# Kernel tuning notes

Hardware: AMD Instinct MI355X
Metric: run time of the kernel (lower is better)

Reference implementation:

```python
import jax, jax.numpy as jnp
import numpy as np
from jax import lax

B, C, H, W = 4, 256, 128, 128
NH = 8
HD = C // NH  # 32
K = 7         # toodd(7) -> 7
DIL = 2
NBH = K // 2  # neighborhood radius


def _window_start(i, L, k, d):
    nh = k // 2
    if d <= 1:
        return max(i - nh, 0) + (L - i - nh - 1 if i + nh >= L else 0)
    ni = i - nh * d
    if ni < 0:
        return i % d
    if i + nh * d >= L:
        imodd = i % d
        a = (L // d) * d
        b = L - a
        if imodd < b:
            return L - b + imodd - 2 * nh * d
        return a + imodd - k * d
    return ni


def _pb_start(i, L, k, d):
    nh = k // 2
    if d <= 1:
        return nh + (nh - i if i < nh else 0) + (L - i - 1 - nh if i + nh >= L else 0)
    if i - nh * d < 0:
        return k - 1 - (i // d)
    if i + nh * d >= L:
        return (L - i - 1) // d
    return nh


# [L, K] neighbor indices per axis, and [L] relative-position-bias start offsets
IDX_H = np.array([[_window_start(i, H, K, DIL) + ki * DIL for ki in range(K)] for i in range(H)], dtype=np.int32)
IDX_W = np.array([[_window_start(j, W, K, DIL) + kj * DIL for kj in range(K)] for j in range(W)], dtype=np.int32)
PB_H = np.array([_pb_start(i, H, K, DIL) for i in range(H)], dtype=np.int32)
PB_W = np.array([_pb_start(j, W, K, DIL) for j in range(W)], dtype=np.int32)


def setup_inputs() -> dict:
    key = jax.random.key(0)
    ks = jax.random.split(key, 8)
    gain = 2.0 ** (-2.5)
    x = jax.random.normal(ks[0], (B, C, H, W), jnp.float32)
    # rotary tables in [-1, 1]
    sin = jax.random.uniform(ks[1], (H, W, HD), jnp.float32, minval=-1.0, maxval=1.0)
    cos = jax.random.uniform(ks[2], (H, W, HD), jnp.float32, minval=-1.0, maxval=1.0)
    w_qkv = jax.random.normal(ks[3], (3 * C, C), jnp.float32) * gain * (2.0 / (4 * C)) ** 0.5
    b_qkv = jnp.zeros((3 * C,), jnp.float32)
    w_lepe = jax.random.normal(ks[4], (C, 1, 5, 5), jnp.float32) * 0.02
    b_lepe = jnp.zeros((C,), jnp.float32)
    w_proj = jax.random.normal(ks[5], (C, C), jnp.float32) * gain * (1.0 / C) ** 0.5
    b_proj = jnp.zeros((C,), jnp.float32)
    rpb = jax.random.normal(ks[6], (NH, 2 * K - 1, 2 * K - 1), jnp.float32) * 0.02
    return {"x": x, "sin": sin, "cos": cos, "w_qkv": w_qkv, "b_qkv": b_qkv,
            "w_lepe": w_lepe, "b_lepe": b_lepe, "w_proj": w_proj, "b_proj": b_proj, "rpb": rpb}


def _rotate_every_two(t):
    t1 = t[..., ::2]
    t2 = t[..., 1::2]
    return jnp.stack([-t2, t1], axis=-1).reshape(t.shape)


def _forward(x, sin, cos, w_qkv, b_qkv, w_lepe, b_lepe, w_proj, b_proj, rpb):
    Bx, Cx, Hx, Wx = x.shape
    # 1x1 qkv conv
    qkv = jnp.einsum('oc,bchw->bohw', w_qkv, x) + b_qkv[None, :, None, None]
    v_chan = qkv[:, 2 * Cx:]
    # LePE: depthwise 5x5 conv on v channels
    lepe = lax.conv_general_dilated(v_chan, w_lepe, (1, 1), [(2, 2), (2, 2)],
                                    feature_group_count=Cx,
                                    dimension_numbers=('NCHW', 'OIHW', 'NCHW'))
    lepe = lepe + b_lepe[None, :, None, None]

    def split_heads(t):  # [B, n*c, H, W] -> [B, n, H, W, c]
        return t.reshape(Bx, NH, HD, Hx, Wx).transpose(0, 1, 3, 4, 2)

    q = split_heads(qkv[:, :Cx])
    k = split_heads(qkv[:, Cx:2 * Cx])
    v = split_heads(v_chan)

    q = (q * cos + _rotate_every_two(q) * sin) * (HD ** -0.5)
    k = k * cos + _rotate_every_two(k) * sin

    idx_h = jnp.asarray(IDX_H)
    idx_w = jnp.asarray(IDX_W)
    pb_h = jnp.asarray(PB_H)
    pb_w = jnp.asarray(PB_W)

    # na2d_qk: dilated neighborhood scores + relative position bias
    attn_slices = []
    for ki in range(K):
        kh = jnp.take(k, idx_h[:, ki], axis=2)          # [B,n,H,W,c]
        for kj in range(K):
            khw = jnp.take(kh, idx_w[:, kj], axis=3)    # [B,n,H,W,c]
            s = jnp.einsum('bnhwc,bnhwc->bnhw', q, khw)
            bias = rpb[:, pb_h + ki][:, :, pb_w + kj]    # [n,H,W]
            attn_slices.append(s + bias[None])
    attn = jnp.stack(attn_slices, axis=-1)               # [B,n,H,W,K*K]
    attn = jax.nn.softmax(attn, axis=-1)

    # na2d_av
    out = jnp.zeros_like(v)
    idx = 0
    for ki in range(K):
        vh = jnp.take(v, idx_h[:, ki], axis=2)
        for kj in range(K):
            vhw = jnp.take(vh, idx_w[:, kj], axis=3)
            out = out + attn[..., idx, None] * vhw
            idx += 1

    out = out.transpose(0, 1, 4, 2, 3).reshape(Bx, Cx, Hx, Wx)  # merge heads
    out = out + lepe
    return jnp.einsum('oc,bchw->bohw', w_proj, out) + b_proj[None, :, None, None]


def reference(x, sin, cos, w_qkv, b_qkv, w_lepe, b_lepe, w_proj, b_proj, rpb):
    return _forward(x, sin, cos, w_qkv, b_qkv, w_lepe, b_lepe, w_proj, b_proj, rpb)
```

## Files before the change

### kernel.cpp

```cpp
#include <hip/hip_runtime.h>
#include <cstddef>

#define HW 16384
#define WID 128

typedef __attribute__((ext_vector_type(8))) short short8;
typedef __attribute__((ext_vector_type(4))) float f32x4;

#define GLD4(g, l)                                                        \
    __builtin_amdgcn_global_load_lds(                                     \
        (const __attribute__((address_space(1))) unsigned int*)(g),       \
        (__attribute__((address_space(3))) unsigned int*)(l), 4, 0, 0)

__device__ __forceinline__ int wstart(int i) {
    if (i < 6) return i & 1;
    if (i >= 122) return 114 + (i & 1);
    return i - 6;
}
__device__ __forceinline__ int pbstart(int i) {
    if (i < 6) return 6 - (i >> 1);
    if (i >= 122) return (127 - i) >> 1;
    return 3;
}

__device__ __forceinline__ unsigned short bf16rne(float f) {
    unsigned u = __builtin_bit_cast(unsigned, f);
    u += 0x7FFFu + ((u >> 16) & 1u);
    return (unsigned short)(u >> 16);
}
__device__ __forceinline__ void bsplit(float f, unsigned short& h, unsigned short& l) {
    h = bf16rne(f);
    float hf = __builtin_bit_cast(float, ((unsigned)h) << 16);
    l = bf16rne(f - hf);
}

template <bool QKV>
__global__ __launch_bounds__(256, 2) void gemm_mfma(
    const float* __restrict__ Wm, const float* __restrict__ Xf, size_t bstr,
    const float* __restrict__ bias, const float* __restrict__ sinp,
    const float* __restrict__ cosp, float* __restrict__ Y, int NMT, int MT) {
    __shared__ unsigned short As_h[128][40], As_l[128][40];
    __shared__ unsigned short Bs_h[128][40], Bs_l[128][40];
    const int bid = blockIdx.x;
    const int xcd = bid & 7, r = bid >> 3;
    const int mt = r % NMT;
    const int q2 = r / NMT;
    const int nt = xcd * 16 + (q2 & 15);
    const int b = q2 >> 4;
    const int t = threadIdx.x;
    const int lane = t & 63, wid = t >> 6;
    const int wm = wid >> 1, wn = wid & 1;
    const int m0 = mt * 128, n0 = nt * 128;

    f32x4 acc[4][4];
#pragma unroll
    for (int i = 0; i < 4; i++)
#pragma unroll
        for (int j = 0; j < 4; j++) acc[i][j] = (f32x4){0.f, 0.f, 0.f, 0.f};

    const int sr = t >> 1, sh = t & 1;
    const float* arow = Wm + (size_t)(m0 + sr) * 256 + sh * 16;
    const int pl = t & 127, khalf = (t >> 7) * 16;
    const float* xcol = Xf + (size_t)b * bstr + n0 + pl;

    for (int ks = 0; ks < 8; ks++) {
        {
            const float* ap = arow + ks * 32;
#pragma unroll
            for (int g = 0; g < 2; g++) {
                float4 f0 = *(const float4*)(ap + g * 8);
                float4 f1 = *(const float4*)(ap + g * 8 + 4);
                float ff[8] = {f0.x, f0.y, f0.z, f0.w, f1.x, f1.y, f1.z, f1.w};
                short8 vh, vl;
#pragma unroll
                for (int e = 0; e < 8; e++) {
                    unsigned short h, lo_;
                    bsplit(ff[e], h, lo_);
                    vh[e] = (short)h;
                    vl[e] = (short)lo_;
                }
                *(short8*)&As_h[sr][sh * 16 + g * 8] = vh;
                *(short8*)&As_l[sr][sh * 16 + g * 8] = vl;
            }
        }
        {
            const float* xc = xcol + (size_t)(ks * 32 + khalf) * HW;
            float vv[16];
#pragma unroll
            for (int e = 0; e < 16; e++) vv[e] = xc[(size_t)e * HW];
            short8 vh0, vh1, vl0, vl1;
#pragma unroll
            for (int e = 0; e < 8; e++) {
                unsigned short h, lo_;
                bsplit(vv[e], h, lo_);
                vh0[e] = (short)h;
                vl0[e] = (short)lo_;
                bsplit(vv[e + 8], h, lo_);
                vh1[e] = (short)h;
                vl1[e] = (short)lo_;
            }
            *(short8*)&Bs_h[pl][khalf] = vh0;
            *(short8*)&Bs_h[pl][khalf + 8] = vh1;
            *(short8*)&Bs_l[pl][khalf] = vl0;
            *(short8*)&Bs_l[pl][khalf + 8] = vl1;
        }
        __syncthreads();
        const int k8 = (lane >> 4) * 8;
        short8 a_h[4], a_l[4];
#pragma unroll
        for (int mi = 0; mi < 4; mi++) {
            int am = wm * 64 + mi * 16 + (lane & 15);
            a_h[mi] = *(const short8*)&As_h[am][k8];
            a_l[mi] = *(const short8*)&As_l[am][k8];
        }
#pragma unroll
        for (int ni = 0; ni < 4; ni++) {
            int bn = wn * 64 + ni * 16 + (lane & 15);
            short8 b_h = *(const short8*)&Bs_h[bn][k8];
            short8 b_l = *(const short8*)&Bs_l[bn][k8];
#pragma unroll
            for (int mi = 0; mi < 4; mi++) {
                acc[mi][ni] = __builtin_amdgcn_mfma_f32_16x16x32_bf16(a_h[mi], b_h, acc[mi][ni], 0, 0, 0);
                acc[mi][ni] = __builtin_amdgcn_mfma_f32_16x16x32_bf16(a_h[mi], b_l, acc[mi][ni], 0, 0, 0);
                acc[mi][ni] = __builtin_amdgcn_mfma_f32_16x16x32_bf16(a_l[mi], b_h, acc[mi][ni], 0, 0, 0);
            }
        }
        __syncthreads();
    }

    const int col = lane & 15, rq = (lane >> 4) * 4;
    const int s = QKV ? (mt >> 1) : 3;
#pragma unroll
    for (int mi = 0; mi < 4; mi++) {
        int mrow = m0 + wm * 64 + mi * 16 + rq;
        float b0 = bias[mrow], b1 = bias[mrow + 1], b2 = bias[mrow + 2], b3 = bias[mrow + 3];
#pragma unroll
        for (int ni = 0; ni < 4; ni++) {
            int p = n0 + wn * 64 + ni * 16 + col;
            float v0 = acc[mi][ni][0] + b0, v1 = acc[mi][ni][1] + b1;
            float v2 = acc[mi][ni][2] + b2, v3 = acc[mi][ni][3] + b3;
            if (QKV && s < 2) {
                int d0 = (mi & 1) * 16 + rq;
                const float* cp = cosp + (size_t)p * 32 + d0;
                const float* sp = sinp + (size_t)p * 32 + d0;
                float c0 = cp[0], c1 = cp[1], c2 = cp[2], c3 = cp[3];
                float s0 = sp[0], s1 = sp[1], s2 = sp[2], s3 = sp[3];
                float n0_ = v0 * c0 - v1 * s0, n1_ = v1 * c1 + v0 * s1;
                float n2_ = v2 * c2 - v3 * s2, n3_ = v3 * c3 + v2 * s3;
                if (s == 0) {
                    const float scl = 0.17677669529663687f;
                    n0_ *= scl; n1_ *= scl; n2_ *= scl; n3_ *= scl;
                }
                v0 = n0_; v1 = n1_; v2 = n2_; v3 = n3_;
            }
            float* yp = Y + ((size_t)b * MT + mrow) * HW + p;
            yp[0] = v0;
            yp[HW] = v1;
            yp[2 * HW] = v2;
            yp[3 * HW] = v3;
        }
    }
}

#define CW 2048
#define PBUF 4096
__global__ __launch_bounds__(256) void attn_k(const float* __restrict__ qkv,
                                              const float* __restrict__ rpb,
                                              const float* __restrict__ wl,
                                              const float* __restrict__ bl,
                                              float* __restrict__ out) {
    __shared__ float sm[2 * PBUF];
    const int t = threadIdx.x;
    const int ty = t >> 7;
    const int j = t & 127;
    const int bx = blockIdx.x;
    const int ip = ((bx & 7) << 3) | (bx >> 3);
    const int i0 = ip * 2;
    const int i = i0 + ty;
    const int n = blockIdx.y, b = blockIdx.z;
    const int r0 = wstart(i0);
    const int w64 = (t >> 6) * 64;

    const float* qb = qkv + ((size_t)b * 768 + n * 32) * HW;
    const float* kb = qb + (size_t)256 * HW;
    const float* vb = qb + (size_t)512 * HW;
    const int p = i * WID + j;
    const float* qrow = qb + i0 * WID;
    const float* krow = kb + r0 * WID;
    const float* vrow = vb + r0 * WID;

    const int hs = wstart(i), ws_ = wstart(j);
    const int ph = pbstart(i), pw = pbstart(j);

    float sc[49];
    const float* rp = rpb + n * 169;
#pragma unroll
    for (int ki = 0; ki < 7; ki++)
#pragma unroll
        for (int kj = 0; kj < 7; kj++)
            sc[ki * 7 + kj] = rp[(ph + ki) * 13 + (pw + kj)];

    const int aoff = (hs - r0) * WID + ws_;

#pragma unroll
    for (int s = 0; s < 2; s++) {
        const float* kp = krow + (size_t)s * HW;
#pragma unroll
        for (int u = 0; u < 7; u++) GLD4(kp + u * 256 + t, &sm[s * CW + u * 256 + w64]);
        GLD4(qrow + (size_t)s * HW + t, &sm[s * CW + 1792 + w64]);
    }

    for (int cp = 0; cp < 16; cp++) {
        float* bc = sm + (cp & 1) * PBUF;
        float* bnx = sm + ((cp + 1) & 1) * PBUF;
        if (cp < 15) {
#pragma unroll
            for (int s = 0; s < 2; s++) {
                const int c = 2 * (cp + 1) + s;
                const float* kp = krow + (size_t)c * HW;
#pragma unroll
                for (int u = 0; u < 7; u++) GLD4(kp + u * 256 + t, &bnx[s * CW + u * 256 + w64]);
                GLD4(qrow + (size_t)c * HW + t, &bnx[s * CW + 1792 + w64]);
            }
            asm volatile("s_waitcnt vmcnt(16)" ::: "memory");
        } else {
#pragma unroll
            for (int s = 0; s < 2; s++) {
                const float* vp = vrow + (size_t)s * HW;
#pragma unroll
                for (int u = 0; u < 7; u++) GLD4(vp + u * 256 + t, &bnx[s * CW + u * 256 + w64]);
            }
            asm volatile("s_waitcnt vmcnt(14)" ::: "memory");
        }
        __builtin_amdgcn_s_barrier();
        __builtin_amdgcn_s_setprio(1);
#pragma unroll
        for (int s = 0; s < 2; s++) {
            const float* bs = bc + s * CW;
            float qc = bs[1792 + t];
            const float* smb = bs + aoff;
#pragma unroll
            for (int ki = 0; ki < 7; ki++) {
                const float* kib = smb + ki * 256;
#pragma unroll
                for (int kj = 0; kj < 7; kj++)
                    sc[ki * 7 + kj] = fmaf(qc, kib[kj * 2], sc[ki * 7 + kj]);
            }
        }
        __builtin_amdgcn_s_setprio(0);
        __builtin_amdgcn_s_barrier();
    }

    float mx = sc[0];
#pragma unroll
    for (int u = 1; u < 49; u++) mx = fmaxf(mx, sc[u]);
    float sum = 0.0f;
#pragma unroll
    for (int u = 0; u < 49; u++) {
        sc[u] = __expf(sc[u] - mx);
        sum += sc[u];
    }
    float inv = 1.0f / sum;
#pragma unroll
    for (int u = 0; u < 49; u++) sc[u] *= inv;

    float* ob = out + ((size_t)b * 768 + n * 32) * HW + p;
    const float* wbase = wl + (size_t)(n * 32) * 25;
    const float* blb = bl + n * 32;
    for (int cp = 0; cp < 16; cp++) {
        float* bc = sm + (cp & 1) * PBUF;
        float* bnx = sm + ((cp + 1) & 1) * PBUF;
        if (cp < 15) {
#pragma unroll
            for (int s = 0; s < 2; s++) {
                const int c = 2 * (cp + 1) + s;
                const float* vp = vrow + (size_t)c * HW;
#pragma unroll
                for (int u = 0; u < 7; u++) GLD4(vp + u * 256 + t, &bnx[s * CW + u * 256 + w64]);
            }
            asm volatile("s_waitcnt vmcnt(14)" ::: "memory");
        } else {
            asm volatile("s_waitcnt vmcnt(0)" ::: "memory");
        }
        __builtin_amdgcn_s_barrier();
        __builtin_amdgcn_s_setprio(1);
#pragma unroll
        for (int s = 0; s < 2; s++) {
            const int ch = 2 * cp + s;
            const float* bs = bc + s * CW;
            const float* smb = bs + aoff;
            float oc = 0.0f;
#pragma unroll
            for (int ki = 0; ki < 7; ki++) {
                const float* kib = smb + ki * 256;
#pragma unroll
                for (int kj = 0; kj < 7; kj++)
                    oc = fmaf(sc[ki * 7 + kj], kib[kj * 2], oc);
            }
            const float* wrow = wbase + ch * 25;
            float lac = blb[ch];
#pragma unroll
            for (int di = 0; di < 5; di++) {
                int ii = i + di - 2;
                if ((unsigned)ii < 128u) {
                    const float* srow = bs + (ii - r0) * WID;
                    const float* wr = wrow + di * 5;
#pragma unroll
                    for (int dj = 0; dj < 5; dj++) {
                        int jj = j + dj - 2;
                        if ((unsigned)jj < 128u)
                            lac = fmaf(wr[dj], srow[jj], lac);
                    }
                }
            }
            ob[(size_t)ch * HW] = oc + lac;
        }
        __builtin_amdgcn_s_setprio(0);
        __builtin_amdgcn_s_barrier();
    }
}

extern "C" void kernel_launch(void* const* d_in, const int* in_sizes, int n_in,
                              void* d_out, int out_size, void* d_ws, size_t ws_size,
                              hipStream_t stream) {
    const float* x = (const float*)d_in[0];
    const float* sinp = (const float*)d_in[1];
    const float* cosp = (const float*)d_in[2];
    const float* w_qkv = (const float*)d_in[3];
    const float* b_qkv = (const float*)d_in[4];
    const float* w_lepe = (const float*)d_in[5];
    const float* b_lepe = (const float*)d_in[6];
    const float* w_proj = (const float*)d_in[7];
    const float* b_proj = (const float*)d_in[8];
    const float* rpb = (const float*)d_in[9];
    float* out = (float*)d_out;

    float* qkvb = (float*)d_ws;

    gemm_mfma<true><<<dim3(3072), 256, 0, stream>>>(w_qkv, x, (size_t)256 * HW, b_qkv,
                                                    sinp, cosp, qkvb, 6, 768);
    attn_k<<<dim3(64, 8, 4), 256, 0, stream>>>(qkvb, rpb, w_lepe, b_lepe, qkvb);
    gemm_mfma<false><<<dim3(1024), 256, 0, stream>>>(w_proj, qkvb, (size_t)768 * HW, b_proj,
                                                     nullptr, nullptr, out, 2, 256);
}
```

Before: 369.6 us.

## Compute two output rows per thread in attention kernel to reuse K/V window rows

The attention kernel now has each thread handle two query rows (i and i+2), so each block covers four rows and the grid halves. The staged K/V window grows from 7 to 8 rows, and rows shared by both dilated neighborhoods are loaded from LDS once and used for both accumulations. This applies to scores, PV and the LePE conv. Q is now read straight into registers instead of being staged through LDS. The cost is doubled score registers (98 floats) with a launch-bounds hint of 3 blocks per CU, which risks spills, plus half as many blocks; the bf16 split helper also switches to HIP intrinsics.

```diff
diff --git a/kernel.cpp b/kernel.cpp
--- a/kernel.cpp
+++ b/kernel.cpp
@@ -1,4 +1,5 @@
 #include <hip/hip_runtime.h>
+#include <hip/hip_bf16.h>
 #include <cstddef>
 
 #define HW 16384
@@ -23,15 +24,11 @@
     return 3;
 }
 
-__device__ __forceinline__ unsigned short bf16rne(float f) {
-    unsigned u = __builtin_bit_cast(unsigned, f);
-    u += 0x7FFFu + ((u >> 16) & 1u);
-    return (unsigned short)(u >> 16);
-}
 __device__ __forceinline__ void bsplit(float f, unsigned short& h, unsigned short& l) {
-    h = bf16rne(f);
-    float hf = __builtin_bit_cast(float, ((unsigned)h) << 16);
-    l = bf16rne(f - hf);
+    __hip_bfloat16 hb = __float2bfloat16(f);
+    h = __builtin_bit_cast(unsigned short, hb);
+    float hf = __bfloat162float(hb);
+    l = __builtin_bit_cast(unsigned short, __float2bfloat16(f - hf));
 }
 
 template <bool QKV>
@@ -162,158 +159,213 @@
     }
 }
 
-#define CW 2048
-#define PBUF 4096
-__global__ __launch_bounds__(256) void attn_k(const float* __restrict__ qkv,
-                                              const float* __restrict__ rpb,
-                                              const float* __restrict__ wl,
-                                              const float* __restrict__ bl,
-                                              float* __restrict__ out) {
-    __shared__ float sm[2 * PBUF];
+template <int O>
+__device__ __forceinline__ void qk2(const float* win, int aoff, float qA, float qB,
+                                    float (&sl)[49], float (&sh)[49]) {
+    const float* rw = win + aoff;
+#pragma unroll
+    for (int u = 0; u < 7 + O; u++) {
+        float tp[7];
+#pragma unroll
+        for (int kj = 0; kj < 7; kj++) tp[kj] = rw[kj * 2];
+        if (u < 7) {
+#pragma unroll
+            for (int kj = 0; kj < 7; kj++) sl[u * 7 + kj] = fmaf(qA, tp[kj], sl[u * 7 + kj]);
+        }
+        if (u >= O) {
+#pragma unroll
+            for (int kj = 0; kj < 7; kj++) sh[(u - O) * 7 + kj] = fmaf(qB, tp[kj], sh[(u - O) * 7 + kj]);
+        }
+        rw += 2 * WID;
+    }
+}
+
+template <int O>
+__device__ __forceinline__ void pv2(const float* win, int aoff, const float (&sl)[49],
+                                    const float (&sh)[49], float& oA, float& oB) {
+    const float* rw = win + aoff;
+#pragma unroll
+    for (int u = 0; u < 7 + O; u++) {
+        float tp[7];
+#pragma unroll
+        for (int kj = 0; kj < 7; kj++) tp[kj] = rw[kj * 2];
+        if (u < 7) {
+#pragma unroll
+            for (int kj = 0; kj < 7; kj++) oA = fmaf(sl[u * 7 + kj], tp[kj], oA);
+        }
+        if (u >= O) {
+#pragma unroll
+            for (int kj = 0; kj < 7; kj++) oB = fmaf(sh[(u - O) * 7 + kj], tp[kj], oB);
+        }
+        rw += 2 * WID;
+    }
+}
+
+#define CWIN 2048
+#define PB2 4096
+__global__ __launch_bounds__(256, 3) void attn_k(const float* __restrict__ qkv,
+                                                 const float* __restrict__ rpb,
+                                                 const float* __restrict__ wl,
+                                                 const float* __restrict__ bl,
+                                                 float* __restrict__ out) {
+    __shared__ float sm[2 * PB2];
     const int t = threadIdx.x;
     const int ty = t >> 7;
     const int j = t & 127;
     const int bx = blockIdx.x;
-    const int ip = ((bx & 7) << 3) | (bx >> 3);
-    const int i0 = ip * 2;
+    const int it = ((bx & 7) << 2) | (bx >> 3);
+    const int n = blockIdx.y, b = blockIdx.z;
+    const int i0 = it * 4;
     const int i = i0 + ty;
-    const int n = blockIdx.y, b = blockIdx.z;
     const int r0 = wstart(i0);
     const int w64 = (t >> 6) * 64;
 
     const float* qb = qkv + ((size_t)b * 768 + n * 32) * HW;
     const float* kb = qb + (size_t)256 * HW;
     const float* vb = qb + (size_t)512 * HW;
-    const int p = i * WID + j;
-    const float* qrow = qb + i0 * WID;
-    const float* krow = kb + r0 * WID;
-    const float* vrow = vb + r0 * WID;
+    const int pA = i * WID + j;
+    const int pB = pA + 2 * WID;
+
+    int woff[8];
+#pragma unroll
+    for (int u = 0; u < 8; u++) {
+        int row = r0 + 2 * u + ty;
+        if (row > 127) row = 127;
+        woff[u] = row * WID + j;
+    }
 
     const int hs = wstart(i), ws_ = wstart(j);
-    const int ph = pbstart(i), pw = pbstart(j);
-
-    float sc[49];
-    const float* rp = rpb + n * 169;
-#pragma unroll
-    for (int ki = 0; ki < 7; ki++)
-#pragma unroll
-        for (int kj = 0; kj < 7; kj++)
-            sc[ki * 7 + kj] = rp[(ph + ki) * 13 + (pw + kj)];
-
+    const int O1 = (wstart(i + 2) - hs) >> 1;
     const int aoff = (hs - r0) * WID + ws_;
 
+    float sl[49], sh[49];
+    {
+        const float* rp = rpb + n * 169;
+        const int phA = pbstart(i), phB = pbstart(i + 2), pw = pbstart(j);
+#pragma unroll
+        for (int ki = 0; ki < 7; ki++)
+#pragma unroll
+            for (int kj = 0; kj < 7; kj++) {
+                sl[ki * 7 + kj] = rp[(phA + ki) * 13 + (pw + kj)];
+                sh[ki * 7 + kj] = rp[(phB + ki) * 13 + (pw + kj)];
+            }
+    }
+
 #pragma unroll
     for (int s = 0; s < 2; s++) {
-        const float* kp = krow + (size_t)s * HW;
-#pragma unroll
-        for (int u = 0; u < 7; u++) GLD4(kp + u * 256 + t, &sm[s * CW + u * 256 + w64]);
-        GLD4(qrow + (size_t)s * HW + t, &sm[s * CW + 1792 + w64]);
-    }
+        const float* kp = kb + (size_t)s * HW;
+#pragma unroll
+        for (int u = 0; u < 8; u++) GLD4(kp + woff[u], &sm[s * CWIN + u * 256 + w64]);
+    }
+    float qA0 = qb[pA], qB0 = qb[pB];
+    float qA1 = qb[HW + pA], qB1 = qb[HW + pB];
 
     for (int cp = 0; cp < 16; cp++) {
-        float* bc = sm + (cp & 1) * PBUF;
-        float* bnx = sm + ((cp + 1) & 1) * PBUF;
+        const float* bc = sm + (cp & 1) * PB2;
+        float* bnx = sm + ((cp + 1) & 1) * PB2;
+        float qnA0 = 0.f, qnB0 = 0.f, qnA1 = 0.f, qnB1 = 0.f;
         if (cp < 15) {
 #pragma unroll
             for (int s = 0; s < 2; s++) {
-                const int c = 2 * (cp + 1) + s;
-                const float* kp = krow + (size_t)c * HW;
-#pragma unroll
-                for (int u = 0; u < 7; u++) GLD4(kp + u * 256 + t, &bnx[s * CW + u * 256 + w64]);
-                GLD4(qrow + (size_t)c * HW + t, &bnx[s * CW + 1792 + w64]);
+                const float* kp = kb + (size_t)(2 * (cp + 1) + s) * HW;
+#pragma unroll
+                for (int u = 0; u < 8; u++) GLD4(kp + woff[u], &bnx[s * CWIN + u * 256 + w64]);
+            }
+            qnA0 = qb[(size_t)(2 * cp + 2) * HW + pA];
+            qnB0 = qb[(size_t)(2 * cp + 2) * HW + pB];
+            qnA1 = qb[(size_t)(2 * cp + 3) * HW + pA];
+            qnB1 = qb[(size_t)(2 * cp + 3) * HW + pB];
+            asm volatile("s_waitcnt vmcnt(20)" ::: "memory");
+        } else {
+#pragma unroll
+            for (int s = 0; s < 2; s++) {
+                const float* vp = vb + (size_t)s * HW;
+#pragma unroll
+                for (int u = 0; u < 8; u++) GLD4(vp + woff[u], &bnx[s * CWIN + u * 256 + w64]);
+            }
+            asm volatile("s_waitcnt vmcnt(16)" ::: "memory");
+        }
+        __builtin_amdgcn_s_barrier();
+        __builtin_amdgcn_s_setprio(1);
+        if (O1) {
+            qk2<1>(bc, aoff, qA0, qB0, sl, sh);
+            qk2<1>(bc + CWIN, aoff, qA1, qB1, sl, sh);
+        } else {
+            qk2<0>(bc, aoff, qA0, qB0, sl, sh);
+            qk2<0>(bc + CWIN, aoff, qA1, qB1, sl, sh);
+        }
+        __builtin_amdgcn_s_setprio(0);
+        qA0 = qnA0; qB0 = qnB0; qA1 = qnA1; qB1 = qnB1;
+        __builtin_amdgcn_s_barrier();
+    }
+
+    float mx0 = sl[0], mx1 = sh[0];
+#pragma unroll
+    for (int u = 1; u < 49; u++) {
+        mx0 = fmaxf(mx0, sl[u]);
+        mx1 = fmaxf(mx1, sh[u]);
+    }
+    float s0 = 0.f, s1 = 0.f;
+#pragma unroll
+    for (int u = 0; u < 49; u++) {
+        sl[u] = __expf(sl[u] - mx0); s0 += sl[u];
+        sh[u] = __expf(sh[u] - mx1); s1 += sh[u];
+    }
+    float inv0 = 1.f / s0, inv1 = 1.f / s1;
+#pragma unroll
+    for (int u = 0; u < 49; u++) {
+        sl[u] *= inv0;
+        sh[u] *= inv1;
+    }
+
+    float* ob = out + ((size_t)b * 768 + n * 32) * HW;
+    const float* wlb = wl + (size_t)(n * 32) * 25;
+    const float* blb = bl + n * 32;
+    for (int cp = 0; cp < 16; cp++) {
+        const float* bc = sm + (cp & 1) * PB2;
+        float* bnx = sm + ((cp + 1) & 1) * PB2;
+        if (cp < 15) {
+#pragma unroll
+            for (int s = 0; s < 2; s++) {
+                const float* vp = vb + (size_t)(2 * (cp + 1) + s) * HW;
+#pragma unroll
+                for (int u = 0; u < 8; u++) GLD4(vp + woff[u], &bnx[s * CWIN + u * 256 + w64]);
             }
             asm volatile("s_waitcnt vmcnt(16)" ::: "memory");
         } else {
-#pragma unroll
-            for (int s = 0; s < 2; s++) {
-                const float* vp = vrow + (size_t)s * HW;
-#pragma unroll
-                for (int u = 0; u < 7; u++) GLD4(vp + u * 256 + t, &bnx[s * CW + u * 256 + w64]);
-            }
-            asm volatile("s_waitcnt vmcnt(14)" ::: "memory");
+            asm volatile("s_waitcnt vmcnt(0)" ::: "memory");
         }
         __builtin_amdgcn_s_barrier();
         __builtin_amdgcn_s_setprio(1);
 #pragma unroll
         for (int s = 0; s < 2; s++) {
-            const float* bs = bc + s * CW;
-            float qc = bs[1792 + t];
-            const float* smb = bs + aoff;
-#pragma unroll
-            for (int ki = 0; ki < 7; ki++) {
-                const float* kib = smb + ki * 256;
-#pragma unroll
-                for (int kj = 0; kj < 7; kj++)
-                    sc[ki * 7 + kj] = fmaf(qc, kib[kj * 2], sc[ki * 7 + kj]);
-            }
-        }
-        __builtin_amdgcn_s_setprio(0);
-        __builtin_amdgcn_s_barrier();
-    }
-
-    float mx = sc[0];
-#pragma unroll
-    for (int u = 1; u < 49; u++) mx = fmaxf(mx, sc[u]);
-    float sum = 0.0f;
-#pragma unroll
-    for (int u = 0; u < 49; u++) {
-        sc[u] = __expf(sc[u] - mx);
-        sum += sc[u];
-    }
-    float inv = 1.0f / sum;
-#pragma unroll
-    for (int u = 0; u < 49; u++) sc[u] *= inv;
-
-    float* ob = out + ((size_t)b * 768 + n * 32) * HW + p;
-    const float* wbase = wl + (size_t)(n * 32) * 25;
-    const float* blb = bl + n * 32;
-    for (int cp = 0; cp < 16; cp++) {
-        float* bc = sm + (cp & 1) * PBUF;
-        float* bnx = sm + ((cp + 1) & 1) * PBUF;
-        if (cp < 15) {
-#pragma unroll
-            for (int s = 0; s < 2; s++) {
-                const int c = 2 * (cp + 1) + s;
-                const float* vp = vrow + (size_t)c * HW;
-#pragma unroll
-                for (int u = 0; u < 7; u++) GLD4(vp + u * 256 + t, &bnx[s * CW + u * 256 + w64]);
-            }
-            asm volatile("s_waitcnt vmcnt(14)" ::: "memory");
-        } else {
-            asm volatile("s_waitcnt vmcnt(0)" ::: "memory");
-        }
-        __builtin_amdgcn_s_barrier();
-        __builtin_amdgcn_s_setprio(1);
-#pragma unroll
-        for (int s = 0; s < 2; s++) {
             const int ch = 2 * cp + s;
-            const float* bs = bc + s * CW;
-            const float* smb = bs + aoff;
-            float oc = 0.0f;
-#pragma unroll
-            for (int ki = 0; ki < 7; ki++) {
-                const float* kib = smb + ki * 256;
-#pragma unroll
-                for (int kj = 0; kj < 7; kj++)
-                    oc = fmaf(sc[ki * 7 + kj], kib[kj * 2], oc);
-            }
-            const float* wrow = wbase + ch * 25;
-            float lac = blb[ch];
-#pragma unroll
-            for (int di = 0; di < 5; di++) {
-                int ii = i + di - 2;
+            const float* win = bc + s * CWIN;
+            float oA = 0.f, oB = 0.f;
+            if (O1) pv2<1>(win, aoff, sl, sh, oA, oB);
+            else    pv2<0>(win, aoff, sl, sh, oA, oB);
+            const float* wrow = wlb + ch * 25;
+            float lA = blb[ch], lB = lA;
+            const float* wb2 = win + (i - 2 - r0) * WID + (j - 2);
+#pragma unroll
+            for (int dd = 0; dd < 7; dd++) {
+                int ii = i - 2 + dd;
                 if ((unsigned)ii < 128u) {
-                    const float* srow = bs + (ii - r0) * WID;
-                    const float* wr = wrow + di * 5;
+                    const float* srow = wb2 + dd * WID;
 #pragma unroll
                     for (int dj = 0; dj < 5; dj++) {
-                        int jj = j + dj - 2;
-                        if ((unsigned)jj < 128u)
-                            lac = fmaf(wr[dj], srow[jj], lac);
+                        int jj = j - 2 + dj;
+                        if ((unsigned)jj < 128u) {
+                            float tv = srow[dj];
+                            if (dd <= 4) lA = fmaf(wrow[dd * 5 + dj], tv, lA);
+                            if (dd >= 2) lB = fmaf(wrow[(dd - 2) * 5 + dj], tv, lB);
+                        }
                     }
                 }
             }
-            ob[(size_t)ch * HW] = oc + lac;
+            float* op = ob + (size_t)ch * HW;
+            op[pA] = oA + lA;
+            op[pB] = oB + lB;
         }
         __builtin_amdgcn_s_setprio(0);
         __builtin_amdgcn_s_barrier();
@@ -339,7 +391,7 @@
 
     gemm_mfma<true><<<dim3(3072), 256, 0, stream>>>(w_qkv, x, (size_t)256 * HW, b_qkv,
                                                     sinp, cosp, qkvb, 6, 768);
-    attn_k<<<dim3(64, 8, 4), 256, 0, stream>>>(qkvb, rpb, w_lepe, b_lepe, qkvb);
+    attn_k<<<dim3(32, 8, 4), 256, 0, stream>>>(qkvb, rpb, w_lepe, b_lepe, qkvb);
     gemm_mfma<false><<<dim3(1024), 256, 0, stream>>>(w_proj, qkvb, (size_t)768 * HW, b_proj,
                                                      nullptr, nullptr, out, 2, 256);
 }
```

Measured after the change: 467.6 us. 1.27x slower.
